# Optimization experiments

Hardware: AMD Instinct MI355X
Metric: run time of the kernel (lower is better)

## Reference

```python
import jax, jax.numpy as jnp
import numpy as np

B, N_IN, N_OUT, DEG = 128, 16384, 8192, 64
N_EDGES = N_OUT * DEG


def setup_inputs() -> dict:
    key = jax.random.key(0)
    k_x, k_src, k_dst, k_w = jax.random.split(key, 4)
    x = jax.random.normal(k_x, (B, N_IN), dtype=jnp.float32)
    # Ragged connectivity flattened to a CSR-like edge list:
    # edge_src[e] -> input feature index, edge_dst[e] -> output unit index.
    edge_src = jax.random.randint(k_src, (N_EDGES,), 0, N_IN, dtype=jnp.int64)
    edge_dst = jnp.sort(jax.random.randint(k_dst, (N_EDGES,), 0, N_OUT, dtype=jnp.int64))
    w = jax.random.normal(k_w, (N_EDGES,), dtype=jnp.float32) * 0.05  # one weight per edge
    bias = jnp.zeros((N_OUT,), dtype=jnp.float32)
    return {"x": x, "w": w, "bias": bias, "edge_src": edge_src, "edge_dst": edge_dst}


def reference(x, w, bias, edge_src, edge_dst):
    # Equivalent to: for each output j, y[:, j] = relu(x[:, edges_j] @ w_j + bias[j])
    # Vectorized as a single gather + weighted scatter-add over the flat edge list.
    n_out = bias.shape[0]
    gathered = x[:, edge_src] * w  # [B, E]
    y = jnp.zeros((x.shape[0], n_out), dtype=x.dtype).at[:, edge_dst].add(gathered)
    return jax.nn.relu(y + bias)
```

## Files before the change

kernel.cpp:

```cpp
#include <hip/hip_runtime.h>

#define B_DIM   128
#define N_IN    16384
#define N_OUT   8192
#define N_EDGES (N_OUT * 64)

#define WAVES_PB 8
#define J_BLK    WAVES_PB
#define THREADS  (WAVES_PB * 64)

#define CHUNKB   32
#define NCHUNK   (B_DIM / CHUNKB)
#define JGROUPS  (N_OUT / J_BLK)

__device__ __forceinline__ int lower_bound_dev(const int* __restrict__ a, int n, int v) {
    int lo = 0, hi = n;
    while (lo < hi) {
        int mid = (lo + hi) >> 1;
        if (a[mid] < v) lo = mid + 1; else hi = mid;
    }
    return lo;
}

__global__ void build_rowptr_kernel(const int* __restrict__ dst, int* __restrict__ rp) {
    const int e = blockIdx.x * blockDim.x + threadIdx.x;
    if (e >= N_EDGES) return;
    const int d     = dst[e];
    const int dprev = (e == 0) ? -1 : dst[e - 1];
    for (int j = dprev + 1; j <= d; ++j) rp[j] = e;
    if (e == N_EDGES - 1)
        for (int j = d + 1; j <= N_OUT; ++j) rp[j] = N_EDGES;
}

__global__ __launch_bounds__(256) void transpose_kernel(const float* __restrict__ x,
                                                        float* __restrict__ xT) {
    __shared__ float tile[32][33];
    const int i0 = blockIdx.x * 32;
    const int b0 = blockIdx.y * 32;
    const int tx = threadIdx.x;
    const int ty = threadIdx.y;
#pragma unroll
    for (int r = 0; r < 32; r += 8)
        tile[ty + r][tx] = x[(size_t)(b0 + ty + r) * N_IN + (i0 + tx)];
    __syncthreads();
#pragma unroll
    for (int r = 0; r < 32; r += 8)
        xT[(size_t)(i0 + ty + r) * B_DIM + (b0 + tx)] = tile[tx][ty + r];
}

__global__ __launch_bounds__(THREADS, 8) void sparse_layer_chunked(
        const float* __restrict__ xT, const float* __restrict__ w,
        const float* __restrict__ bias, const int* __restrict__ src,
        const int* __restrict__ rp, float* __restrict__ y) {
    __shared__ float tile[J_BLK][36];

    const int tid   = threadIdx.x;
    const int wid   = tid >> 6;
    const int lane  = tid & 63;
    const int slot  = lane >> 3;
    const int bl    = lane & 7;
    const int chunk = blockIdx.x >> 10;
    const int jg    = blockIdx.x & (JGROUPS - 1);
    const int cb    = chunk * CHUNKB;
    const int j0    = jg * J_BLK;
    const int j     = j0 + wid;

    const int e0 = __builtin_amdgcn_readfirstlane(rp[j]);
    const int e1 = __builtin_amdgcn_readfirstlane(rp[j + 1]);

    float4 acc = {0.f, 0.f, 0.f, 0.f};
    const float* xbase = xT + cb + 4 * bl;

#pragma unroll 2
    for (int e = e0; e < e1; e += 8) {
        const int  ee    = e + slot;
        const bool valid = ee < e1;
        const int  ec    = valid ? ee : e0;
        const int  s     = src[ec];
        const float wt   = valid ? w[ec] : 0.f;
        const float4 v   = *(const float4*)(xbase + (size_t)s * B_DIM);
        acc.x = fmaf(v.x, wt, acc.x);
        acc.y = fmaf(v.y, wt, acc.y);
        acc.z = fmaf(v.z, wt, acc.z);
        acc.w = fmaf(v.w, wt, acc.w);
    }

#pragma unroll
    for (int m = 8; m <= 32; m <<= 1) {
        acc.x += __shfl_xor(acc.x, m, 64);
        acc.y += __shfl_xor(acc.y, m, 64);
        acc.z += __shfl_xor(acc.z, m, 64);
        acc.w += __shfl_xor(acc.w, m, 64);
    }

    if (slot == 0) {
        *(float4*)&tile[wid][4 * bl] = acc;
    }
    __syncthreads();

    if (tid < J_BLK * CHUNKB) {
        const int jj = tid & (J_BLK - 1);
        const int bb = tid >> 3;
        const float v = tile[jj][bb] + bias[j0 + jj];
        y[(size_t)(cb + bb) * N_OUT + (j0 + jj)] = fmaxf(v, 0.f);
    }
}

__global__ __launch_bounds__(THREADS) void sparse_layer_fallback(
        const float* __restrict__ x, const float* __restrict__ w,
        const float* __restrict__ bias, const int* __restrict__ src,
        const int* __restrict__ dst, float* __restrict__ y) {
    __shared__ float tile[J_BLK][130];
    __shared__ int   srp[J_BLK + 1];

    const int tid  = threadIdx.x;
    const int wid  = tid >> 6;
    const int lane = tid & 63;
    const int j0   = blockIdx.x * J_BLK;

    if (tid <= J_BLK) srp[tid] = lower_bound_dev(dst, N_EDGES, j0 + tid);
    __syncthreads();

    const int e0 = srp[wid], e1 = srp[wid + 1];
    const int b0 = lane * 2;
    float acc0 = 0.f, acc1 = 0.f;
    for (int e = e0; e < e1; ++e) {
        const int   s  = src[e];
        const float wt = w[e];
        acc0 = fmaf(x[(size_t)b0 * N_IN + s], wt, acc0);
        acc1 = fmaf(x[(size_t)(b0 + 1) * N_IN + s], wt, acc1);
    }
    tile[wid][b0]     = acc0;
    tile[wid][b0 + 1] = acc1;
    __syncthreads();
#pragma unroll
    for (int i = tid; i < B_DIM * J_BLK; i += THREADS) {
        const int bb = i >> 3;
        const int jj = i & (J_BLK - 1);
        const float v = tile[jj][bb] + bias[j0 + jj];
        y[(size_t)bb * N_OUT + (j0 + jj)] = fmaxf(v, 0.f);
    }
}

extern "C" void kernel_launch(void* const* d_in, const int* in_sizes, int n_in,
                              void* d_out, int out_size, void* d_ws, size_t ws_size,
                              hipStream_t stream) {
    const float* x    = (const float*)d_in[0];
    const float* w    = (const float*)d_in[1];
    const float* bias = (const float*)d_in[2];
    const int*   esrc = (const int*)d_in[3];
    const int*   edst = (const int*)d_in[4];
    float*       y    = (float*)d_out;

    const size_t RP_BYTES = (size_t)(N_OUT + 1) * sizeof(int);
    const size_t XT_OFF   = 65536;
    const size_t XT_BYTES = (size_t)N_IN * B_DIM * sizeof(float);

    const bool has_ws = ws_size >= XT_OFF + XT_BYTES && ws_size >= RP_BYTES;

    int*   rp = (int*)d_ws;
    float* xT = (float*)((char*)d_ws + XT_OFF);

    if (has_ws) {
        build_rowptr_kernel<<<(N_EDGES + 255) / 256, 256, 0, stream>>>(edst, rp);
        transpose_kernel<<<dim3(N_IN / 32, B_DIM / 32), dim3(32, 8), 0, stream>>>(x, xT);
        sparse_layer_chunked<<<dim3(JGROUPS * NCHUNK), THREADS, 0, stream>>>(xT, w, bias, esrc, rp, y);
    } else {
        sparse_layer_fallback<<<dim3(N_OUT / J_BLK), THREADS, 0, stream>>>(x, w, bias, esrc, edst, y);
    }
}
```

Before: 100.2 us.

## Store transposed activations in fp16 and gather full batch per edge

The transpose kernel now writes x transposed as half precision, which halves the workspace footprint and the bytes moved by each gathered row. The sparse kernel drops the four batch-chunk split: each wave handles all 128 batch entries, reading 16 bytes (8 halves) per lane across 4 edges per step and accumulating in fp32. This cuts the number of blocks fourfold and removes redundant index and weight loads across chunks, but it adds fp16 rounding error on x, which may exceed the tolerance.

```diff
diff --git a/kernel.cpp b/kernel.cpp
--- a/kernel.cpp
+++ b/kernel.cpp
@@ -1,16 +1,13 @@
 #include <hip/hip_runtime.h>
+#include <hip/hip_fp16.h>
 
 #define B_DIM   128
 #define N_IN    16384
 #define N_OUT   8192
 #define N_EDGES (N_OUT * 64)
 
-#define WAVES_PB 8
-#define J_BLK    WAVES_PB
-#define THREADS  (WAVES_PB * 64)
-
-#define CHUNKB   32
-#define NCHUNK   (B_DIM / CHUNKB)
+#define J_BLK    8
+#define THREADS  (J_BLK * 64)
 #define JGROUPS  (N_OUT / J_BLK)
 
 __device__ __forceinline__ int lower_bound_dev(const int* __restrict__ a, int n, int v) {
@@ -32,77 +29,81 @@
         for (int j = d + 1; j <= N_OUT; ++j) rp[j] = N_EDGES;
 }
 
-__global__ __launch_bounds__(256) void transpose_kernel(const float* __restrict__ x,
-                                                        float* __restrict__ xT) {
-    __shared__ float tile[32][33];
+__global__ __launch_bounds__(256) void transpose_h_kernel(const float* __restrict__ x,
+                                                          __half* __restrict__ xTh) {
+    __shared__ float tile[64][33];
     const int i0 = blockIdx.x * 32;
-    const int b0 = blockIdx.y * 32;
+    const int b0 = blockIdx.y * 64;
     const int tx = threadIdx.x;
     const int ty = threadIdx.y;
 #pragma unroll
-    for (int r = 0; r < 32; r += 8)
+    for (int r = 0; r < 64; r += 8)
         tile[ty + r][tx] = x[(size_t)(b0 + ty + r) * N_IN + (i0 + tx)];
     __syncthreads();
+    __half2* out = (__half2*)xTh;
 #pragma unroll
-    for (int r = 0; r < 32; r += 8)
-        xT[(size_t)(i0 + ty + r) * B_DIM + (b0 + tx)] = tile[tx][ty + r];
+    for (int rr = 0; rr < 4; ++rr) {
+        const int il = rr * 8 + ty;
+        const float a = tile[2 * tx][il];
+        const float b = tile[2 * tx + 1][il];
+        out[(size_t)(i0 + il) * (B_DIM / 2) + (b0 >> 1) + tx] = __floats2half2_rn(a, b);
+    }
 }
 
-__global__ __launch_bounds__(THREADS, 8) void sparse_layer_chunked(
-        const float* __restrict__ xT, const float* __restrict__ w,
+__global__ __launch_bounds__(THREADS, 8) void sparse_layer_h(
+        const __half* __restrict__ xTh, const float* __restrict__ w,
         const float* __restrict__ bias, const int* __restrict__ src,
         const int* __restrict__ rp, float* __restrict__ y) {
-    __shared__ float tile[J_BLK][36];
+    __shared__ float tile[J_BLK][132];
 
-    const int tid   = threadIdx.x;
-    const int wid   = tid >> 6;
-    const int lane  = tid & 63;
-    const int slot  = lane >> 3;
-    const int bl    = lane & 7;
-    const int chunk = blockIdx.x >> 10;
-    const int jg    = blockIdx.x & (JGROUPS - 1);
-    const int cb    = chunk * CHUNKB;
-    const int j0    = jg * J_BLK;
-    const int j     = j0 + wid;
+    const int tid  = threadIdx.x;
+    const int wid  = tid >> 6;
+    const int lane = tid & 63;
+    const int slot = lane >> 4;
+    const int bl   = lane & 15;
+    const int j0   = blockIdx.x * J_BLK;
+    const int j    = j0 + wid;
 
     const int e0 = __builtin_amdgcn_readfirstlane(rp[j]);
     const int e1 = __builtin_amdgcn_readfirstlane(rp[j + 1]);
 
-    float4 acc = {0.f, 0.f, 0.f, 0.f};
-    const float* xbase = xT + cb + 4 * bl;
+    float acc[8] = {0.f, 0.f, 0.f, 0.f, 0.f, 0.f, 0.f, 0.f};
+    const char* xbase = (const char*)xTh + bl * 16;
 
-#pragma unroll 2
-    for (int e = e0; e < e1; e += 8) {
+#pragma unroll 4
+    for (int e = e0; e < e1; e += 4) {
         const int  ee    = e + slot;
         const bool valid = ee < e1;
         const int  ec    = valid ? ee : e0;
         const int  s     = src[ec];
         const float wt   = valid ? w[ec] : 0.f;
-        const float4 v   = *(const float4*)(xbase + (size_t)s * B_DIM);
-        acc.x = fmaf(v.x, wt, acc.x);
-        acc.y = fmaf(v.y, wt, acc.y);
-        acc.z = fmaf(v.z, wt, acc.z);
-        acc.w = fmaf(v.w, wt, acc.w);
+        const float4 raw = *(const float4*)(xbase + (size_t)s * (B_DIM * 2));
+        const __half2* hp = (const __half2*)&raw;
+#pragma unroll
+        for (int q = 0; q < 4; ++q) {
+            const float2 f = __half22float2(hp[q]);
+            acc[2 * q]     = fmaf(f.x, wt, acc[2 * q]);
+            acc[2 * q + 1] = fmaf(f.y, wt, acc[2 * q + 1]);
+        }
     }
 
 #pragma unroll
-    for (int m = 8; m <= 32; m <<= 1) {
-        acc.x += __shfl_xor(acc.x, m, 64);
-        acc.y += __shfl_xor(acc.y, m, 64);
-        acc.z += __shfl_xor(acc.z, m, 64);
-        acc.w += __shfl_xor(acc.w, m, 64);
-    }
+    for (int m = 16; m <= 32; m <<= 1)
+#pragma unroll
+        for (int q = 0; q < 8; ++q) acc[q] += __shfl_xor(acc[q], m, 64);
 
     if (slot == 0) {
-        *(float4*)&tile[wid][4 * bl] = acc;
+#pragma unroll
+        for (int q = 0; q < 8; ++q) tile[wid][8 * bl + q] = acc[q];
     }
     __syncthreads();
 
-    if (tid < J_BLK * CHUNKB) {
-        const int jj = tid & (J_BLK - 1);
-        const int bb = tid >> 3;
+#pragma unroll
+    for (int i = tid; i < B_DIM * J_BLK; i += THREADS) {
+        const int bb = i >> 3;
+        const int jj = i & (J_BLK - 1);
         const float v = tile[jj][bb] + bias[j0 + jj];
-        y[(size_t)(cb + bb) * N_OUT + (j0 + jj)] = fmaxf(v, 0.f);
+        y[(size_t)bb * N_OUT + (j0 + jj)] = fmaxf(v, 0.f);
     }
 }
 
@@ -154,17 +155,17 @@
 
     const size_t RP_BYTES = (size_t)(N_OUT + 1) * sizeof(int);
     const size_t XT_OFF   = 65536;
-    const size_t XT_BYTES = (size_t)N_IN * B_DIM * sizeof(float);
+    const size_t XT_BYTES = (size_t)N_IN * B_DIM * sizeof(__half);
 
     const bool has_ws = ws_size >= XT_OFF + XT_BYTES && ws_size >= RP_BYTES;
 
-    int*   rp = (int*)d_ws;
-    float* xT = (float*)((char*)d_ws + XT_OFF);
+    int*    rp  = (int*)d_ws;
+    __half* xTh = (__half*)((char*)d_ws + XT_OFF);
 
     if (has_ws) {
         build_rowptr_kernel<<<(N_EDGES + 255) / 256, 256, 0, stream>>>(edst, rp);
-        transpose_kernel<<<dim3(N_IN / 32, B_DIM / 32), dim3(32, 8), 0, stream>>>(x, xT);
-        sparse_layer_chunked<<<dim3(JGROUPS * NCHUNK), THREADS, 0, stream>>>(xT, w, bias, esrc, rp, y);
+        transpose_h_kernel<<<dim3(N_IN / 32, B_DIM / 64), dim3(32, 8), 0, stream>>>(x, xTh);
+        sparse_layer_h<<<dim3(JGROUPS), THREADS, 0, stream>>>(xTh, w, bias, esrc, rp, y);
     } else {
         sparse_layer_fallback<<<dim3(N_OUT / J_BLK), THREADS, 0, stream>>>(x, w, bias, esrc, edst, y);
     }
```

New measurement: 86.77 us. 13.4% less time.
